# Kernel tuning notes

Measured on AMD Instinct MI355X. Metric: run time of the kernel, lower is better.

## Reference

```python
import jax, jax.numpy as jnp
import numpy as np

DILATIONS = [1, 2, 4, 8, 16, 32, 64, 128, 256, 1, 2, 4, 8, 16, 32, 64, 128, 256]
KSIZE = 3
CHAN = 16
NUM_SIG = 1       # num_channels in original
NUM_CTRL = 3      # control channels appended to signal
FRAME_SIZE = 2048
R = sum(d * (KSIZE - 1) for d in DILATIONS) + 1  # 2045
BATCH = 64
T = FRAME_SIZE + R - 1  # 4092


def causal_conv1d(x, w, b, dil):
    # x: [B,T,Cin], w: [K,Cin,Cout] (Keras layout), causal left pad dil*(K-1)
    pad = dil * (w.shape[0] - 1)
    y = jax.lax.conv_general_dilated(
        x, w, window_strides=(1,), padding=[(pad, 0)],
        rhs_dilation=(dil,), dimension_numbers=("NWC", "WIO", "NWC"))
    return y + b


def setup_inputs() -> dict:
    key = jax.random.key(0)
    ks = jax.random.split(key, 8)
    n_layers = len(DILATIONS)
    in0 = NUM_SIG + NUM_CTRL            # layer 0 sees 1 signal + 3 controls = 4
    in_rest = CHAN + NUM_CTRL           # layers 1.. see 16-ch signal + 3 controls = 19
    s = 0.1
    inp = {
        "input": jax.random.normal(ks[0], (BATCH, T, in0), dtype=jnp.float32),
        "conv_w0": jax.random.normal(ks[1], (KSIZE, in0, CHAN), dtype=jnp.float32) * s,
        "conv_w": jax.random.normal(ks[2], (n_layers - 1, KSIZE, in_rest, CHAN), dtype=jnp.float32) * s,
        "conv_b": jax.random.normal(ks[3], (n_layers, CHAN), dtype=jnp.float32) * s,
        "io_w": jax.random.normal(ks[4], (n_layers - 1, CHAN, CHAN), dtype=jnp.float32) * s,
        "io_b": jax.random.normal(ks[5], (n_layers - 1, CHAN), dtype=jnp.float32) * s,
        "mixer_w": jax.random.normal(ks[6], (n_layers * CHAN, NUM_SIG), dtype=jnp.float32) * s,
        "mixer_b": jax.random.normal(ks[7], (NUM_SIG,), dtype=jnp.float32) * s,
    }
    return inp


def reference(input, conv_w0, conv_w, conv_b, io_w, io_b, mixer_w, mixer_b):
    signal = input[:, :, :NUM_SIG]        # [B,T,1]
    controls = input[:, :, NUM_SIG:]      # [B,T,3]
    n_layers = len(DILATIONS)
    acc = []
    for i in range(n_layers):
        w = conv_w0 if i == 0 else conv_w[i - 1]
        h = jnp.concatenate([signal, controls], axis=2)
        h = causal_conv1d(h, w, conv_b[i], DILATIONS[i])
        h = jax.nn.relu(h)                # [B,T,16]
        acc.append(h)
        if i != n_layers - 1:
            # 1x1 conv residual mix + halved channel-sum skip of previous signal
            signal = (jnp.einsum("btc,co->bto", h, io_w[i]) + io_b[i]
                      + jnp.sum(signal, axis=2, keepdims=True) / 2)
    accumulator = jnp.concatenate(acc, axis=2)  # [B,T,288]
    mixed = jnp.einsum("btc,co->bto", accumulator, mixer_w) + mixer_b
    return mixed[:, -FRAME_SIZE:, :]
```

## Files before the change

### kernel.cpp

```cpp
#include <hip/hip_runtime.h>

#define TFULL 4092
#define NB    64
#define CH    16
#define OUT_T 2048
#define TOFF  2044
#define NT    512
#define RSTRIDE 20

template<int L0, int NL, int TILE, int HALO, bool FIRSTG, bool LASTG>
__global__ __launch_bounds__(NT, 4) void group_kernel(
    const float* __restrict__ input,
    const float* __restrict__ conv_w0,
    const float* __restrict__ conv_w,
    const float* __restrict__ conv_b,
    const float* __restrict__ io_w,
    const float* __restrict__ io_b,
    const float* __restrict__ mixer_w,
    const float* __restrict__ mixer_b,
    const float* __restrict__ sig_in,
    float* __restrict__ sig_out,
    float* __restrict__ out,
    int out_start)
{
    constexpr int NROWS = TILE + HALO;
    __shared__ float buf[NROWS * RSTRIDE];
    __shared__ float macc[TILE];

    const int b       = blockIdx.y;
    const int tile_lo = out_start + blockIdx.x * TILE;
    const int tile_hi = (tile_lo + TILE < TFULL) ? (tile_lo + TILE) : TFULL;
    const int buf_lo  = tile_lo - HALO;
    const int tid     = threadIdx.x;

    {
        const float* ib = input + ((size_t)b * TFULL + buf_lo) * 4;
        const int nstage = tile_hi - buf_lo;
        for (int j = tid; j < nstage; j += NT) {
            *(float4*)(&buf[j * RSTRIDE + 16]) = *(const float4*)(ib + (size_t)j * 4);
            if constexpr (!FIRSTG) {
                const float* sp = sig_in + ((size_t)b * TFULL + (buf_lo + j)) * CH;
                *(float4*)(&buf[j * RSTRIDE + 0])  = *(const float4*)(sp + 0);
                *(float4*)(&buf[j * RSTRIDE + 4])  = *(const float4*)(sp + 4);
                *(float4*)(&buf[j * RSTRIDE + 8])  = *(const float4*)(sp + 8);
                *(float4*)(&buf[j * RSTRIDE + 12]) = *(const float4*)(sp + 12);
            }
        }
        for (int j = tid; j < TILE; j += NT) macc[j] = 0.f;
    }
    __syncthreads();

    int lo = buf_lo;
    for (int i = 0; i < NL; ++i) {
        const int g   = L0 + i;
        const int dil = 1 << (g % 9);
        lo += 2 * dil;
        const bool lastl = (i == NL - 1);
        const float* wb   = (FIRSTG && g == 0) ? conv_w0 : (conv_w + (size_t)(g - 1) * 3 * 19 * CH);
        const float* bias = conv_b  + (size_t)g * CH;
        const float* iw   = io_w    + (size_t)g * CH * CH;
        const float* iob2 = io_b    + (size_t)g * CH;
        const float* mw   = mixer_w + (size_t)g * CH;

        const int n   = tile_hi - lo;
        const int nch = (n + NT - 1) / NT;
        for (int c = 0; c < nch; ++c) {
            const int r   = tile_hi - (c + 1) * NT + tid;
            const bool act = (r >= lo);
            int j = 0;
            float sn[CH];
            if (act) {
                j = r - buf_lo;
                const float* r2 = &buf[j * RSTRIDE];
                const float* r1 = &buf[(j - dil) * RSTRIDE];
                const float* r0 = &buf[(j - 2 * dil) * RSTRIDE];

                float h[CH];
                #pragma unroll
                for (int o = 0; o < CH; ++o) h[o] = bias[o];
                float sum_t;

                if (FIRSTG && g == 0) {
                    const float4 x0 = *(const float4*)(r0 + 16);
                    const float4 x1 = *(const float4*)(r1 + 16);
                    const float4 x2 = *(const float4*)(r2 + 16);
                    const float t0[4] = {x0.x, x0.y, x0.z, x0.w};
                    const float t1[4] = {x1.x, x1.y, x1.z, x1.w};
                    const float t2[4] = {x2.x, x2.y, x2.z, x2.w};
                    #pragma unroll
                    for (int cc = 0; cc < 4; ++cc) {
                        #pragma unroll
                        for (int o = 0; o < CH; ++o) {
                            h[o] = fmaf(t0[cc], wb[(0 * 4 + cc) * CH + o], h[o]);
                            h[o] = fmaf(t1[cc], wb[(1 * 4 + cc) * CH + o], h[o]);
                            h[o] = fmaf(t2[cc], wb[(2 * 4 + cc) * CH + o], h[o]);
                        }
                    }
                    sum_t = x2.x;
                } else {
                    const float4 a0 = *(const float4*)(r0 + 0),  a1 = *(const float4*)(r0 + 4),
                                 a2 = *(const float4*)(r0 + 8),  a3 = *(const float4*)(r0 + 12),
                                 a4 = *(const float4*)(r0 + 16);
                    const float4 b0 = *(const float4*)(r1 + 0),  b1 = *(const float4*)(r1 + 4),
                                 b2 = *(const float4*)(r1 + 8),  b3 = *(const float4*)(r1 + 12),
                                 b4 = *(const float4*)(r1 + 16);
                    const float4 c0 = *(const float4*)(r2 + 0),  c1 = *(const float4*)(r2 + 4),
                                 c2 = *(const float4*)(r2 + 8),  c3 = *(const float4*)(r2 + 12),
                                 c4 = *(const float4*)(r2 + 16);
                    const float t0[19] = {a0.x,a0.y,a0.z,a0.w, a1.x,a1.y,a1.z,a1.w,
                                          a2.x,a2.y,a2.z,a2.w, a3.x,a3.y,a3.z,a3.w,
                                          a4.y,a4.z,a4.w};
                    const float t1[19] = {b0.x,b0.y,b0.z,b0.w, b1.x,b1.y,b1.z,b1.w,
                                          b2.x,b2.y,b2.z,b2.w, b3.x,b3.y,b3.z,b3.w,
                                          b4.y,b4.z,b4.w};
                    const float t2[19] = {c0.x,c0.y,c0.z,c0.w, c1.x,c1.y,c1.z,c1.w,
                                          c2.x,c2.y,c2.z,c2.w, c3.x,c3.y,c3.z,c3.w,
                                          c4.y,c4.z,c4.w};
                    #pragma unroll
                    for (int cc = 0; cc < 19; ++cc) {
                        #pragma unroll
                        for (int o = 0; o < CH; ++o) {
                            h[o] = fmaf(t0[cc], wb[(0 * 19 + cc) * CH + o], h[o]);
                            h[o] = fmaf(t1[cc], wb[(1 * 19 + cc) * CH + o], h[o]);
                            h[o] = fmaf(t2[cc], wb[(2 * 19 + cc) * CH + o], h[o]);
                        }
                    }
                    sum_t = ((c0.x + c0.y) + (c0.z + c0.w)) + ((c1.x + c1.y) + (c1.z + c1.w))
                          + ((c2.x + c2.y) + (c2.z + c2.w)) + ((c3.x + c3.y) + (c3.z + c3.w));
                }
                #pragma unroll
                for (int o = 0; o < CH; ++o) h[o] = fmaxf(h[o], 0.f);

                if (r >= tile_lo && r >= TOFF) {
                    float m = 0.f;
                    #pragma unroll
                    for (int o = 0; o < CH; ++o) m = fmaf(h[o], mw[o], m);
                    macc[r - tile_lo] += m;
                }

                if (!(LASTG && lastl)) {
                    const float half = 0.5f * sum_t;
                    #pragma unroll
                    for (int o = 0; o < CH; ++o) sn[o] = iob2[o] + half;
                    #pragma unroll
                    for (int cc = 0; cc < CH; ++cc) {
                        #pragma unroll
                        for (int o = 0; o < CH; ++o)
                            sn[o] = fmaf(h[cc], iw[cc * CH + o], sn[o]);
                    }
                }
            }
            __syncthreads();
            if (act) {
                if (!lastl) {
                    float* wp = &buf[j * RSTRIDE];
                    *(float4*)(wp + 0)  = make_float4(sn[0],  sn[1],  sn[2],  sn[3]);
                    *(float4*)(wp + 4)  = make_float4(sn[4],  sn[5],  sn[6],  sn[7]);
                    *(float4*)(wp + 8)  = make_float4(sn[8],  sn[9],  sn[10], sn[11]);
                    *(float4*)(wp + 12) = make_float4(sn[12], sn[13], sn[14], sn[15]);
                } else if (!LASTG) {
                    float* gp = sig_out + ((size_t)b * TFULL + r) * CH;
                    *(float4*)(gp + 0)  = make_float4(sn[0],  sn[1],  sn[2],  sn[3]);
                    *(float4*)(gp + 4)  = make_float4(sn[4],  sn[5],  sn[6],  sn[7]);
                    *(float4*)(gp + 8)  = make_float4(sn[8],  sn[9],  sn[10], sn[11]);
                    *(float4*)(gp + 12) = make_float4(sn[12], sn[13], sn[14], sn[15]);
                }
            }
        }
        __syncthreads();
    }

    const int nmain = tile_hi - tile_lo;
    for (int j = tid; j < nmain; j += NT) {
        const int r = tile_lo + j;
        if (r >= TOFF) {
            const size_t oi = (size_t)b * OUT_T + (r - TOFF);
            if (FIRSTG) out[oi] = mixer_b[0] + macc[j];
            else        out[oi] += macc[j];
        }
    }
}

template<bool LASTL>
__global__ __launch_bounds__(256, 4) void single_layer(
    const float* __restrict__ input,
    const float* __restrict__ sig_in,
    const float* __restrict__ w,
    const float* __restrict__ bias,
    const float* __restrict__ iw,
    const float* __restrict__ iob,
    const float* __restrict__ mw,
    float* __restrict__ sig_out,
    float* __restrict__ out,
    int dil, int t0)
{
    const int b = blockIdx.y;
    const int t = t0 + blockIdx.x * 256 + threadIdx.x;
    if (t >= TFULL) return;
    const float* ib = input  + (size_t)b * TFULL * 4;
    const float* sb = sig_in + (size_t)b * TFULL * CH;

    const int tt0 = t - 2 * dil, tt1 = t - dil;
    const float4* sp0 = (const float4*)(sb + (size_t)tt0 * CH);
    const float4* sp1 = (const float4*)(sb + (size_t)tt1 * CH);
    const float4* sp2 = (const float4*)(sb + (size_t)t   * CH);
    const float4 a0 = sp0[0], a1 = sp0[1], a2 = sp0[2], a3 = sp0[3];
    const float4 b0 = sp1[0], b1 = sp1[1], b2 = sp1[2], b3 = sp1[3];
    const float4 c0 = sp2[0], c1 = sp2[1], c2 = sp2[2], c3 = sp2[3];
    const float4 x0 = *(const float4*)(ib + (size_t)tt0 * 4);
    const float4 x1 = *(const float4*)(ib + (size_t)tt1 * 4);
    const float4 x2 = *(const float4*)(ib + (size_t)t   * 4);

    float h[CH];
    #pragma unroll
    for (int o = 0; o < CH; ++o) h[o] = bias[o];

    const float t0v[19] = {a0.x,a0.y,a0.z,a0.w, a1.x,a1.y,a1.z,a1.w,
                           a2.x,a2.y,a2.z,a2.w, a3.x,a3.y,a3.z,a3.w,
                           x0.y,x0.z,x0.w};
    const float t1v[19] = {b0.x,b0.y,b0.z,b0.w, b1.x,b1.y,b1.z,b1.w,
                           b2.x,b2.y,b2.z,b2.w, b3.x,b3.y,b3.z,b3.w,
                           x1.y,x1.z,x1.w};
    const float t2v[19] = {c0.x,c0.y,c0.z,c0.w, c1.x,c1.y,c1.z,c1.w,
                           c2.x,c2.y,c2.z,c2.w, c3.x,c3.y,c3.z,c3.w,
                           x2.y,x2.z,x2.w};
    #pragma unroll
    for (int cc = 0; cc < 19; ++cc) {
        #pragma unroll
        for (int o = 0; o < CH; ++o) {
            h[o] = fmaf(t0v[cc], w[(0 * 19 + cc) * CH + o], h[o]);
            h[o] = fmaf(t1v[cc], w[(1 * 19 + cc) * CH + o], h[o]);
            h[o] = fmaf(t2v[cc], w[(2 * 19 + cc) * CH + o], h[o]);
        }
    }
    #pragma unroll
    for (int o = 0; o < CH; ++o) h[o] = fmaxf(h[o], 0.f);

    if (t >= TOFF) {
        float m = 0.f;
        #pragma unroll
        for (int o = 0; o < CH; ++o) m = fmaf(h[o], mw[o], m);
        out[(size_t)b * OUT_T + (t - TOFF)] += m;
    }

    if constexpr (!LASTL) {
        const float sum_t = ((c0.x + c0.y) + (c0.z + c0.w)) + ((c1.x + c1.y) + (c1.z + c1.w))
                          + ((c2.x + c2.y) + (c2.z + c2.w)) + ((c3.x + c3.y) + (c3.z + c3.w));
        float sn[CH];
        const float half = 0.5f * sum_t;
        #pragma unroll
        for (int o = 0; o < CH; ++o) sn[o] = iob[o] + half;
        #pragma unroll
        for (int cc = 0; cc < CH; ++cc) {
            #pragma unroll
            for (int o = 0; o < CH; ++o)
                sn[o] = fmaf(h[cc], iw[cc * CH + o], sn[o]);
        }
        float* gp = sig_out + ((size_t)b * TFULL + t) * CH;
        *(float4*)(gp + 0)  = make_float4(sn[0],  sn[1],  sn[2],  sn[3]);
        *(float4*)(gp + 4)  = make_float4(sn[4],  sn[5],  sn[6],  sn[7]);
        *(float4*)(gp + 8)  = make_float4(sn[8],  sn[9],  sn[10], sn[11]);
        *(float4*)(gp + 12) = make_float4(sn[12], sn[13], sn[14], sn[15]);
    }
}

extern "C" void kernel_launch(void* const* d_in, const int* in_sizes, int n_in,
                              void* d_out, int out_size, void* d_ws, size_t ws_size,
                              hipStream_t stream) {
    const float* input   = (const float*)d_in[0];
    const float* conv_w0 = (const float*)d_in[1];
    const float* conv_w  = (const float*)d_in[2];
    const float* conv_b  = (const float*)d_in[3];
    const float* io_w    = (const float*)d_in[4];
    const float* io_b    = (const float*)d_in[5];
    const float* mixer_w = (const float*)d_in[6];
    const float* mixer_b = (const float*)d_in[7];
    float* out = (float*)d_out;

    float* s1 = (float*)d_ws;
    float* s2 = s1 + (size_t)NB * TFULL * CH;

    auto wl  = [&](int g) { return conv_w + (size_t)(g - 1) * 3 * 19 * CH; };
    auto bsl = [&](int g) { return conv_b + (size_t)g * CH; };
    auto iwl = [&](int g) { return io_w + (size_t)g * CH * CH; };
    auto ibl = [&](int g) { return io_b + (size_t)g * CH; };
    auto mwl = [&](int g) { return mixer_w + (size_t)g * CH; };

    dim3 blk512(NT, 1, 1), blk256(256, 1, 1);

    group_kernel<0, 7, 480, 254, true, false><<<dim3(8, NB), blk512, 0, stream>>>(
        input, conv_w0, conv_w, conv_b, io_w, io_b, mixer_w, mixer_b,
        nullptr, s1, out, 254);
    single_layer<false><<<dim3(14, NB), blk256, 0, stream>>>(
        input, s1, wl(7), bsl(7), iwl(7), ibl(7), mwl(7), s2, out, 128, 510);
    single_layer<false><<<dim3(12, NB), blk256, 0, stream>>>(
        input, s2, wl(8), bsl(8), iwl(8), ibl(8), mwl(8), s1, out, 256, 1022);
    group_kernel<9, 6, 368, 126, false, false><<<dim3(8, NB), blk512, 0, stream>>>(
        input, conv_w0, conv_w, conv_b, io_w, io_b, mixer_w, mixer_b,
        s1, s2, out, 1148);
    single_layer<false><<<dim3(11, NB), blk256, 0, stream>>>(
        input, s2, wl(15), bsl(15), iwl(15), ibl(15), mwl(15), s1, out, 64, 1276);
    single_layer<false><<<dim3(10, NB), blk256, 0, stream>>>(
        input, s1, wl(16), bsl(16), iwl(16), ibl(16), mwl(16), s2, out, 128, 1532);
    single_layer<true><<<dim3(8, NB), blk256, 0, stream>>>(
        input, s2, wl(17), bsl(17), nullptr, nullptr, mwl(17), nullptr, out, 256, 2044);
}
```

Before: 334.5 us.

## Restructure group kernel with planar LDS, register accumulators, and fused layers 9-16

Rewrites the layer-group kernel to keep the signal in four float4 planes in shared memory and to read the control inputs directly from global memory instead of staging them. Each thread now owns exactly two fixed rows, which removes the shared mixer accumulator and the per-chunk loop. The second group now covers eight layers (9-16), which removes two separate single-layer launches and their global round trips, at the cost of more halo recomputation. The group kernel now assumes a tile plus halo of at most 1024 rows.

```diff
diff --git a/kernel.cpp b/kernel.cpp
--- a/kernel.cpp
+++ b/kernel.cpp
@@ -5,11 +5,10 @@
 #define CH    16
 #define OUT_T 2048
 #define TOFF  2044
-#define NT    512
-#define RSTRIDE 20
-
-template<int L0, int NL, int TILE, int HALO, bool FIRSTG, bool LASTG>
-__global__ __launch_bounds__(NT, 4) void group_kernel(
+#define GNT   512
+
+template<int L0, int NL, int TILE, int HALO, bool FIRSTG>
+__global__ __launch_bounds__(GNT, 4) void group2_kernel(
     const float* __restrict__ input,
     const float* __restrict__ conv_w0,
     const float* __restrict__ conv_w,
@@ -24,159 +23,166 @@
     int out_start)
 {
     constexpr int NROWS = TILE + HALO;
-    __shared__ float buf[NROWS * RSTRIDE];
-    __shared__ float macc[TILE];
+    __shared__ float4 buf4[4][NROWS];
+    float4* pl0 = buf4[0]; float4* pl1 = buf4[1];
+    float4* pl2 = buf4[2]; float4* pl3 = buf4[3];
 
     const int b       = blockIdx.y;
+    const int tid     = threadIdx.x;
     const int tile_lo = out_start + blockIdx.x * TILE;
     const int tile_hi = (tile_lo + TILE < TFULL) ? (tile_lo + TILE) : TFULL;
     const int buf_lo  = tile_lo - HALO;
-    const int tid     = threadIdx.x;
-
-    {
-        const float* ib = input + ((size_t)b * TFULL + buf_lo) * 4;
-        const int nstage = tile_hi - buf_lo;
-        for (int j = tid; j < nstage; j += NT) {
-            *(float4*)(&buf[j * RSTRIDE + 16]) = *(const float4*)(ib + (size_t)j * 4);
-            if constexpr (!FIRSTG) {
-                const float* sp = sig_in + ((size_t)b * TFULL + (buf_lo + j)) * CH;
-                *(float4*)(&buf[j * RSTRIDE + 0])  = *(const float4*)(sp + 0);
-                *(float4*)(&buf[j * RSTRIDE + 4])  = *(const float4*)(sp + 4);
-                *(float4*)(&buf[j * RSTRIDE + 8])  = *(const float4*)(sp + 8);
-                *(float4*)(&buf[j * RSTRIDE + 12]) = *(const float4*)(sp + 12);
-            }
-        }
-        for (int j = tid; j < TILE; j += NT) macc[j] = 0.f;
-    }
-    __syncthreads();
-
-    int lo = buf_lo;
+    const int jmax    = tile_hi - buf_lo;
+    const int j0      = NROWS - 1024 + tid;
+    const int j1      = NROWS - 512 + tid;
+
+    const float4* ib4 = (const float4*)(input + (size_t)b * TFULL * 4);
+
+    if constexpr (!FIRSTG) {
+        const float* sp = sig_in + (size_t)b * TFULL * CH;
+        for (int j = tid; j < jmax; j += GNT) {
+            const float4* row = (const float4*)(sp + (size_t)(buf_lo + j) * CH);
+            pl0[j] = row[0]; pl1[j] = row[1]; pl2[j] = row[2]; pl3[j] = row[3];
+        }
+        __syncthreads();
+    }
+
+    float acc0 = 0.f, acc1 = 0.f;
+    int lo_off = 0;
     for (int i = 0; i < NL; ++i) {
         const int g   = L0 + i;
         const int dil = 1 << (g % 9);
-        lo += 2 * dil;
+        lo_off += 2 * dil;
         const bool lastl = (i == NL - 1);
-        const float* wb   = (FIRSTG && g == 0) ? conv_w0 : (conv_w + (size_t)(g - 1) * 3 * 19 * CH);
+        const float* wb   = (FIRSTG && g == 0) ? conv_w0
+                                               : conv_w + (size_t)(g - 1) * 3 * 19 * CH;
         const float* bias = conv_b  + (size_t)g * CH;
         const float* iw   = io_w    + (size_t)g * CH * CH;
-        const float* iob2 = io_b    + (size_t)g * CH;
+        const float* ob   = io_b    + (size_t)g * CH;
         const float* mw   = mixer_w + (size_t)g * CH;
 
-        const int n   = tile_hi - lo;
-        const int nch = (n + NT - 1) / NT;
-        for (int c = 0; c < nch; ++c) {
-            const int r   = tile_hi - (c + 1) * NT + tid;
-            const bool act = (r >= lo);
-            int j = 0;
-            float sn[CH];
-            if (act) {
-                j = r - buf_lo;
-                const float* r2 = &buf[j * RSTRIDE];
-                const float* r1 = &buf[(j - dil) * RSTRIDE];
-                const float* r0 = &buf[(j - 2 * dil) * RSTRIDE];
-
-                float h[CH];
+        const bool a0 = (j0 >= lo_off) && (j0 < jmax);
+        const bool a1 = (j1 >= lo_off) && (j1 < jmax);
+
+        float sn0[CH], sn1[CH];
+
+        auto row_compute = [&](int j, float* sn, float& accr) {
+            float h[CH];
+            #pragma unroll
+            for (int o = 0; o < CH; ++o) h[o] = bias[o];
+            float sum;
+            if (FIRSTG && g == 0) {
+                const float4 x0 = ib4[buf_lo + j - 2];
+                const float4 x1 = ib4[buf_lo + j - 1];
+                const float4 x2 = ib4[buf_lo + j];
+                const float t0[4] = {x0.x, x0.y, x0.z, x0.w};
+                const float t1[4] = {x1.x, x1.y, x1.z, x1.w};
+                const float t2[4] = {x2.x, x2.y, x2.z, x2.w};
                 #pragma unroll
-                for (int o = 0; o < CH; ++o) h[o] = bias[o];
-                float sum_t;
-
-                if (FIRSTG && g == 0) {
-                    const float4 x0 = *(const float4*)(r0 + 16);
-                    const float4 x1 = *(const float4*)(r1 + 16);
-                    const float4 x2 = *(const float4*)(r2 + 16);
-                    const float t0[4] = {x0.x, x0.y, x0.z, x0.w};
-                    const float t1[4] = {x1.x, x1.y, x1.z, x1.w};
-                    const float t2[4] = {x2.x, x2.y, x2.z, x2.w};
+                for (int cc = 0; cc < 4; ++cc) {
                     #pragma unroll
-                    for (int cc = 0; cc < 4; ++cc) {
-                        #pragma unroll
-                        for (int o = 0; o < CH; ++o) {
-                            h[o] = fmaf(t0[cc], wb[(0 * 4 + cc) * CH + o], h[o]);
-                            h[o] = fmaf(t1[cc], wb[(1 * 4 + cc) * CH + o], h[o]);
-                            h[o] = fmaf(t2[cc], wb[(2 * 4 + cc) * CH + o], h[o]);
-                        }
+                    for (int o = 0; o < CH; ++o) {
+                        h[o] = fmaf(t0[cc], wb[(0 * 4 + cc) * CH + o], h[o]);
+                        h[o] = fmaf(t1[cc], wb[(1 * 4 + cc) * CH + o], h[o]);
+                        h[o] = fmaf(t2[cc], wb[(2 * 4 + cc) * CH + o], h[o]);
                     }
-                    sum_t = x2.x;
-                } else {
-                    const float4 a0 = *(const float4*)(r0 + 0),  a1 = *(const float4*)(r0 + 4),
-                                 a2 = *(const float4*)(r0 + 8),  a3 = *(const float4*)(r0 + 12),
-                                 a4 = *(const float4*)(r0 + 16);
-                    const float4 b0 = *(const float4*)(r1 + 0),  b1 = *(const float4*)(r1 + 4),
-                                 b2 = *(const float4*)(r1 + 8),  b3 = *(const float4*)(r1 + 12),
-                                 b4 = *(const float4*)(r1 + 16);
-                    const float4 c0 = *(const float4*)(r2 + 0),  c1 = *(const float4*)(r2 + 4),
-                                 c2 = *(const float4*)(r2 + 8),  c3 = *(const float4*)(r2 + 12),
-                                 c4 = *(const float4*)(r2 + 16);
-                    const float t0[19] = {a0.x,a0.y,a0.z,a0.w, a1.x,a1.y,a1.z,a1.w,
-                                          a2.x,a2.y,a2.z,a2.w, a3.x,a3.y,a3.z,a3.w,
-                                          a4.y,a4.z,a4.w};
-                    const float t1[19] = {b0.x,b0.y,b0.z,b0.w, b1.x,b1.y,b1.z,b1.w,
-                                          b2.x,b2.y,b2.z,b2.w, b3.x,b3.y,b3.z,b3.w,
-                                          b4.y,b4.z,b4.w};
-                    const float t2[19] = {c0.x,c0.y,c0.z,c0.w, c1.x,c1.y,c1.z,c1.w,
-                                          c2.x,c2.y,c2.z,c2.w, c3.x,c3.y,c3.z,c3.w,
-                                          c4.y,c4.z,c4.w};
+                }
+                sum = x2.x;
+            } else {
+                sum = 0.f;
+                #pragma unroll
+                for (int k = 0; k < 3; ++k) {
+                    const int jm = j - (2 - k) * dil;
+                    const float4 s0 = pl0[jm], s1v = pl1[jm],
+                                 s2v = pl2[jm], s3v = pl3[jm];
+                    const float4 x  = ib4[buf_lo + jm];
+                    const float tv[19] = {s0.x, s0.y, s0.z, s0.w,
+                                          s1v.x, s1v.y, s1v.z, s1v.w,
+                                          s2v.x, s2v.y, s2v.z, s2v.w,
+                                          s3v.x, s3v.y, s3v.z, s3v.w,
+                                          x.y, x.z, x.w};
+                    if (k == 2)
+                        sum = ((s0.x + s0.y) + (s0.z + s0.w))
+                            + ((s1v.x + s1v.y) + (s1v.z + s1v.w))
+                            + ((s2v.x + s2v.y) + (s2v.z + s2v.w))
+                            + ((s3v.x + s3v.y) + (s3v.z + s3v.w));
                     #pragma unroll
                     for (int cc = 0; cc < 19; ++cc) {
                         #pragma unroll
-                        for (int o = 0; o < CH; ++o) {
-                            h[o] = fmaf(t0[cc], wb[(0 * 19 + cc) * CH + o], h[o]);
-                            h[o] = fmaf(t1[cc], wb[(1 * 19 + cc) * CH + o], h[o]);
-                            h[o] = fmaf(t2[cc], wb[(2 * 19 + cc) * CH + o], h[o]);
-                        }
-                    }
-                    sum_t = ((c0.x + c0.y) + (c0.z + c0.w)) + ((c1.x + c1.y) + (c1.z + c1.w))
-                          + ((c2.x + c2.y) + (c2.z + c2.w)) + ((c3.x + c3.y) + (c3.z + c3.w));
-                }
-                #pragma unroll
-                for (int o = 0; o < CH; ++o) h[o] = fmaxf(h[o], 0.f);
-
-                if (r >= tile_lo && r >= TOFF) {
-                    float m = 0.f;
-                    #pragma unroll
-                    for (int o = 0; o < CH; ++o) m = fmaf(h[o], mw[o], m);
-                    macc[r - tile_lo] += m;
-                }
-
-                if (!(LASTG && lastl)) {
-                    const float half = 0.5f * sum_t;
-                    #pragma unroll
-                    for (int o = 0; o < CH; ++o) sn[o] = iob2[o] + half;
-                    #pragma unroll
-                    for (int cc = 0; cc < CH; ++cc) {
-                        #pragma unroll
                         for (int o = 0; o < CH; ++o)
-                            sn[o] = fmaf(h[cc], iw[cc * CH + o], sn[o]);
+                            h[o] = fmaf(tv[cc], wb[(k * 19 + cc) * CH + o], h[o]);
                     }
                 }
             }
+            #pragma unroll
+            for (int o = 0; o < CH; ++o) h[o] = fmaxf(h[o], 0.f);
+
+            const int r = buf_lo + j;
+            if (j >= HALO && r >= TOFF) {
+                float d = 0.f;
+                #pragma unroll
+                for (int o = 0; o < CH; ++o) d = fmaf(h[o], mw[o], d);
+                accr += d;
+            }
+            const float half = 0.5f * sum;
+            #pragma unroll
+            for (int o = 0; o < CH; ++o) sn[o] = ob[o] + half;
+            #pragma unroll
+            for (int cc = 0; cc < CH; ++cc) {
+                #pragma unroll
+                for (int o = 0; o < CH; ++o)
+                    sn[o] = fmaf(h[cc], iw[cc * CH + o], sn[o]);
+            }
+        };
+
+        if (a0) row_compute(j0, sn0, acc0);
+        if (a1) row_compute(j1, sn1, acc1);
+
+        if (!lastl) {
             __syncthreads();
-            if (act) {
-                if (!lastl) {
-                    float* wp = &buf[j * RSTRIDE];
-                    *(float4*)(wp + 0)  = make_float4(sn[0],  sn[1],  sn[2],  sn[3]);
-                    *(float4*)(wp + 4)  = make_float4(sn[4],  sn[5],  sn[6],  sn[7]);
-                    *(float4*)(wp + 8)  = make_float4(sn[8],  sn[9],  sn[10], sn[11]);
-                    *(float4*)(wp + 12) = make_float4(sn[12], sn[13], sn[14], sn[15]);
-                } else if (!LASTG) {
-                    float* gp = sig_out + ((size_t)b * TFULL + r) * CH;
-                    *(float4*)(gp + 0)  = make_float4(sn[0],  sn[1],  sn[2],  sn[3]);
-                    *(float4*)(gp + 4)  = make_float4(sn[4],  sn[5],  sn[6],  sn[7]);
-                    *(float4*)(gp + 8)  = make_float4(sn[8],  sn[9],  sn[10], sn[11]);
-                    *(float4*)(gp + 12) = make_float4(sn[12], sn[13], sn[14], sn[15]);
-                }
-            }
-        }
-        __syncthreads();
-    }
-
-    const int nmain = tile_hi - tile_lo;
-    for (int j = tid; j < nmain; j += NT) {
-        const int r = tile_lo + j;
+            if (a0) {
+                pl0[j0] = make_float4(sn0[0],  sn0[1],  sn0[2],  sn0[3]);
+                pl1[j0] = make_float4(sn0[4],  sn0[5],  sn0[6],  sn0[7]);
+                pl2[j0] = make_float4(sn0[8],  sn0[9],  sn0[10], sn0[11]);
+                pl3[j0] = make_float4(sn0[12], sn0[13], sn0[14], sn0[15]);
+            }
+            if (a1) {
+                pl0[j1] = make_float4(sn1[0],  sn1[1],  sn1[2],  sn1[3]);
+                pl1[j1] = make_float4(sn1[4],  sn1[5],  sn1[6],  sn1[7]);
+                pl2[j1] = make_float4(sn1[8],  sn1[9],  sn1[10], sn1[11]);
+                pl3[j1] = make_float4(sn1[12], sn1[13], sn1[14], sn1[15]);
+            }
+            __syncthreads();
+        } else {
+            if (a0) {
+                float* gp = sig_out + ((size_t)b * TFULL + (buf_lo + j0)) * CH;
+                *(float4*)(gp + 0)  = make_float4(sn0[0],  sn0[1],  sn0[2],  sn0[3]);
+                *(float4*)(gp + 4)  = make_float4(sn0[4],  sn0[5],  sn0[6],  sn0[7]);
+                *(float4*)(gp + 8)  = make_float4(sn0[8],  sn0[9],  sn0[10], sn0[11]);
+                *(float4*)(gp + 12) = make_float4(sn0[12], sn0[13], sn0[14], sn0[15]);
+            }
+            if (a1) {
+                float* gp = sig_out + ((size_t)b * TFULL + (buf_lo + j1)) * CH;
+                *(float4*)(gp + 0)  = make_float4(sn1[0],  sn1[1],  sn1[2],  sn1[3]);
+                *(float4*)(gp + 4)  = make_float4(sn1[4],  sn1[5],  sn1[6],  sn1[7]);
+                *(float4*)(gp + 8)  = make_float4(sn1[8],  sn1[9],  sn1[10], sn1[11]);
+                *(float4*)(gp + 12) = make_float4(sn1[12], sn1[13], sn1[14], sn1[15]);
+            }
+        }
+    }
+
+    if (j0 >= HALO && j0 < jmax) {
+        const int r = buf_lo + j0;
         if (r >= TOFF) {
             const size_t oi = (size_t)b * OUT_T + (r - TOFF);
-            if (FIRSTG) out[oi] = mixer_b[0] + macc[j];
-            else        out[oi] += macc[j];
+            if constexpr (FIRSTG) out[oi] = mixer_b[0] + acc0; else out[oi] += acc0;
+        }
+    }
+    if (j1 >= HALO && j1 < jmax) {
+        const int r = buf_lo + j1;
+        if (r >= TOFF) {
+            const size_t oi = (size_t)b * OUT_T + (r - TOFF);
+            if constexpr (FIRSTG) out[oi] = mixer_b[0] + acc1; else out[oi] += acc1;
         }
     }
 }
@@ -286,22 +292,18 @@
     auto ibl = [&](int g) { return io_b + (size_t)g * CH; };
     auto mwl = [&](int g) { return mixer_w + (size_t)g * CH; };
 
-    dim3 blk512(NT, 1, 1), blk256(256, 1, 1);
-
-    group_kernel<0, 7, 480, 254, true, false><<<dim3(8, NB), blk512, 0, stream>>>(
+    dim3 blkG(GNT, 1, 1), blk256(256, 1, 1);
+
+    group2_kernel<0, 7, 480, 254, true><<<dim3(8, NB), blkG, 0, stream>>>(
         input, conv_w0, conv_w, conv_b, io_w, io_b, mixer_w, mixer_b,
         nullptr, s1, out, 254);
     single_layer<false><<<dim3(14, NB), blk256, 0, stream>>>(
         input, s1, wl(7), bsl(7), iwl(7), ibl(7), mwl(7), s2, out, 128, 510);
     single_layer<false><<<dim3(12, NB), blk256, 0, stream>>>(
         input, s2, wl(8), bsl(8), iwl(8), ibl(8), mwl(8), s1, out, 256, 1022);
-    group_kernel<9, 6, 368, 126, false, false><<<dim3(8, NB), blk512, 0, stream>>>(
+    group2_kernel<9, 8, 320, 510, false><<<dim3(8, NB), blkG, 0, stream>>>(
         input, conv_w0, conv_w, conv_b, io_w, io_b, mixer_w, mixer_b,
-        s1, s2, out, 1148);
-    single_layer<false><<<dim3(11, NB), blk256, 0, stream>>>(
-        input, s2, wl(15), bsl(15), iwl(15), ibl(15), mwl(15), s1, out, 64, 1276);
-    single_layer<false><<<dim3(10, NB), blk256, 0, stream>>>(
-        input, s1, wl(16), bsl(16), iwl(16), ibl(16), mwl(16), s2, out, 128, 1532);
+        s1, s2, out, 1532);
     single_layer<true><<<dim3(8, NB), blk256, 0, stream>>>(
         input, s2, wl(17), bsl(17), nullptr, nullptr, mwl(17), nullptr, out, 256, 2044);
 }
```

New measurement: 306.3 us. 8.4% less time.
